# Optimization experiments

Measured on AMD Instinct MI355X. Metric: run time of the kernel, lower is better.

Reference implementation:

```python
import jax, jax.numpy as jnp
import numpy as np

ALPHA = 0.2  # leaky relu slope

def setup_inputs() -> dict:
    key = jax.random.key(0)
    k1, k2, k3, k4 = jax.random.split(key, 4)
    b, n, din, dout = 8, 2048, 256, 128
    x = jax.random.normal(k1, (b, n, din), dtype=jnp.float32)
    adj = jax.random.randint(k2, (b, n, n), 0, 2, dtype=jnp.int32)
    # xavier-ish scaling for params
    W = jax.random.normal(k3, (dout, din), dtype=jnp.float32) * (1.414 * (2.0 / (din + dout)) ** 0.5)
    a = jax.random.normal(k4, (2 * dout,), dtype=jnp.float32) * (1.414 * (2.0 / (2 * dout + 1)) ** 0.5)
    return {"x": x, "adj": adj, "W": W, "a": a}

def reference(x, adj, W, a):
    # x: [b, n, din]; W: [dout, din]; a: [2*dout]
    wh = jnp.einsum('bnd,od->bno', x, W)           # [b, n, dout]
    dout = W.shape[0]
    a_src, a_dst = a[:dout], a[dout:]
    # e_ij = leaky_relu(a_src . wh_i + a_dst . wh_j)  (decomposed, avoids O(n^2 * 2d) concat)
    e = (wh @ a_src)[:, :, None] + (wh @ a_dst)[:, None, :]  # [b, n, n]
    e = jnp.where(e >= 0, e, ALPHA * e)
    e = jnp.where(adj != 0, e, -jnp.inf)
    attention = jax.nn.softmax(e, axis=2)          # [b, n, n]
    out = jnp.einsum('bij,bjo->bio', attention, wh)  # [b, n, dout]
    return jax.nn.relu(out)
```

## Files before the change

### kernel.cpp

```cpp
#include <hip/hip_runtime.h>
#include <hip/hip_bf16.h>
#include <stdint.h>

#define GAT_ALPHA 0.2f
#define LOG2E 1.4426950408889634f

typedef __attribute__((ext_vector_type(8))) __bf16 bf16x8;
typedef __attribute__((ext_vector_type(4))) float f32x4;

union B8 {
  bf16x8 b;
  unsigned short u[8];
  int4 i4;
};

__device__ __forceinline__ unsigned short f2bf(float f) {
  unsigned int u = __float_as_uint(f);
  u += 0x7fffu + ((u >> 16) & 1u);
  return (unsigned short)(u >> 16);
}

__device__ __forceinline__ void dma16(const void* g, void* l) {
  __builtin_amdgcn_global_load_lds(
      (const __attribute__((address_space(1))) unsigned int*)g,
      (__attribute__((address_space(3))) unsigned int*)l, 16, 0, 0);
}

__global__ __launch_bounds__(256) void gat_pack(
    const int* __restrict__ adj, unsigned long long* __restrict__ mask) {
  const int tid = threadIdx.x;
  const int lane = tid & 63;
  const int wgl = (blockIdx.x * 256 + tid) >> 6;
  for (int it = wgl; it < 131072; it += 4096) {
    const size_t base = (size_t)it << 8;
    const int* p = adj + base + lane;
    int a0 = p[0], a1 = p[64], a2 = p[128], a3 = p[192];
    unsigned long long m0 = __ballot(a0 != 0);
    unsigned long long m1 = __ballot(a1 != 0);
    unsigned long long m2 = __ballot(a2 != 0);
    unsigned long long m3 = __ballot(a3 != 0);
    if (lane == 0) {
      unsigned long long* mp = mask + (base >> 6);
      mp[0] = m0; mp[1] = m1; mp[2] = m2; mp[3] = m3;
    }
  }
}

__global__ __launch_bounds__(256, 2) void gat_wh(
    const float* __restrict__ x, const float* __restrict__ W,
    const float* __restrict__ a, unsigned short* __restrict__ whTf,
    float* __restrict__ s_out, float* __restrict__ d_out) {
  __shared__ float X[32][260];
  __shared__ float Wt[128][68];
  const int tid = threadIdx.x;
  const int row0 = blockIdx.x * 32;
  {
    const int rr = tid >> 3;
    const int seg = (tid & 7) << 2;
    const float* xrow = x + (size_t)(row0 + rr) * 256;
#pragma unroll
    for (int it = 0; it < 8; ++it) {
      const int k = seg + it * 32;
      *(float4*)(&X[rr][k]) = *(const float4*)(xrow + k);
    }
  }
  const int lane32 = tid & 31;
  const int r0 = (tid >> 5) << 2;
  float acc[4][4];
#pragma unroll
  for (int m = 0; m < 4; ++m)
#pragma unroll
    for (int r = 0; r < 4; ++r) acc[m][r] = 0.f;

  for (int kc = 0; kc < 4; ++kc) {
    __syncthreads();
#pragma unroll
    for (int p = 0; p < 8; ++p) {
      const int f = p * 1024 + tid * 4;
      const int row = f >> 6, col = f & 63;
      *(float4*)(&Wt[row][col]) = *(const float4*)(W + row * 256 + kc * 64 + col);
    }
    __syncthreads();
    const int kb = kc << 6;
#pragma unroll
    for (int k4 = 0; k4 < 16; ++k4) {
      const int kk = k4 << 2;
      float4 xv[4], wv[4];
#pragma unroll
      for (int r = 0; r < 4; ++r) xv[r] = *(const float4*)(&X[r0 + r][kb + kk]);
#pragma unroll
      for (int m = 0; m < 4; ++m) wv[m] = *(const float4*)(&Wt[lane32 + 32 * m][kk]);
#pragma unroll
      for (int m = 0; m < 4; ++m)
#pragma unroll
        for (int r = 0; r < 4; ++r) {
          acc[m][r] = fmaf(wv[m].x, xv[r].x, acc[m][r]);
          acc[m][r] = fmaf(wv[m].y, xv[r].y, acc[m][r]);
          acc[m][r] = fmaf(wv[m].z, xv[r].z, acc[m][r]);
          acc[m][r] = fmaf(wv[m].w, xv[r].w, acc[m][r]);
        }
    }
  }
  float asrc[4], adst[4];
#pragma unroll
  for (int m = 0; m < 4; ++m) {
    asrc[m] = a[lane32 + 32 * m];
    adst[m] = a[128 + lane32 + 32 * m];
  }
  float sp[4], dp[4];
#pragma unroll
  for (int r = 0; r < 4; ++r) {
    sp[r] = acc[0][r] * asrc[0] + acc[1][r] * asrc[1] + acc[2][r] * asrc[2] + acc[3][r] * asrc[3];
    dp[r] = acc[0][r] * adst[0] + acc[1][r] * adst[1] + acc[2][r] * adst[2] + acc[3][r] * adst[3];
  }
#pragma unroll
  for (int off = 16; off >= 1; off >>= 1) {
#pragma unroll
    for (int r = 0; r < 4; ++r) {
      sp[r] += __shfl_xor(sp[r], off, 64);
      dp[r] += __shfl_xor(dp[r], off, 64);
    }
  }
  if (lane32 == 0) {
#pragma unroll
    for (int r = 0; r < 4; ++r) {
      s_out[row0 + r0 + r] = sp[r];
      d_out[row0 + r0 + r] = dp[r];
    }
  }
  const int b = row0 >> 11;
  const int jc = (row0 & 2047) >> 5;
  const int q = r0 >> 3;
  const int u0 = r0 & 7;
#pragma unroll
  for (int m = 0; m < 4; ++m) {
    const int o = lane32 + 32 * m;
    const int nt = o >> 4, m16 = o & 15;
    uint2 pk;
    pk.x = (unsigned int)f2bf(acc[m][0]) | ((unsigned int)f2bf(acc[m][1]) << 16);
    pk.y = (unsigned int)f2bf(acc[m][2]) | ((unsigned int)f2bf(acc[m][3]) << 16);
    const size_t addr = ((((size_t)b * 64 + jc) * 8 + nt) << 9) + ((m16 + 16 * q) << 3) + u0;
    *(uint2*)(whTf + addr) = pk;
  }
}

__global__ __launch_bounds__(256) void gat_attn(
    const unsigned int* __restrict__ mask32, const unsigned short* __restrict__ whTf,
    const float* __restrict__ s, const float* __restrict__ dvec,
    float* __restrict__ out) {
  __shared__ unsigned short vbuf[2][2][8][512];
  __shared__ unsigned int maskl[64][68];
  __shared__ float dl[2048];
  const int tid = threadIdx.x;
  const int wave = tid >> 6;
  const int lane = tid & 63;
  const int il = lane & 15;
  const int quad = lane >> 4;
  const int qo = quad << 3;
  const int b = blockIdx.x & 7;
  const int tile = blockIdx.x >> 3;
  const int rbase = tile * 64;
  {
    const float* dsrc = dvec + ((size_t)b << 11);
#pragma unroll
    for (int it = 0; it < 2; ++it) {
      const int idx = it * 1024 + tid * 4;
      *(float4*)(&dl[idx]) = *(const float4*)(dsrc + idx);
    }
  }
  {
    const unsigned int* msrc = mask32 + (((size_t)b << 11) + rbase) * 64;
    const int c4 = (tid & 15) << 2;
#pragma unroll
    for (int kk = 0; kk < 4; ++kk) {
      const int r = (tid >> 4) + kk * 16;
      *(int4*)(&maskl[r][c4]) = *(const int4*)(msrc + r * 64 + c4);
    }
  }
  const unsigned short* whTb = whTf + (((size_t)b * 64) << 12);
  {
#pragma unroll
    for (int h = 0; h < 2; ++h) {
      const int nt = wave * 2 + h;
      dma16(whTb + ((size_t)(0 * 8 + nt) << 9) + (lane << 3), &vbuf[0][0][nt][0]);
      dma16(whTb + ((size_t)(1 * 8 + nt) << 9) + (lane << 3), &vbuf[0][1][nt][0]);
    }
  }
  const int i = rbase + wave * 16 + il;
  const size_t browi = ((size_t)b << 11) + i;
  const float sv = s[browi];
  const int mrow = wave * 16 + il;

  f32x4 acc[8];
#pragma unroll
  for (int nt = 0; nt < 8; ++nt) acc[nt] = (f32x4){0.f, 0.f, 0.f, 0.f};
  float den = 0.f;
  __syncthreads();

#pragma unroll 2
  for (int T = 0; T < 32; ++T) {
    const int cur = T & 1, nxt = cur ^ 1;
    if (T < 31) {
#pragma unroll
      for (int h = 0; h < 2; ++h) {
        const int nt = wave * 2 + h;
        dma16(whTb + (((size_t)(2 * T + 2) * 8 + nt) << 9) + (lane << 3), &vbuf[nxt][0][nt][0]);
        dma16(whTb + (((size_t)(2 * T + 3) * 8 + nt) << 9) + (lane << 3), &vbuf[nxt][1][nt][0]);
      }
    }
#pragma unroll
    for (int c = 0; c < 2; ++c) {
      const int tt = 2 * T + c;
      const int j0 = tt * 32;
      const unsigned int mword = maskl[mrow][tt];
      const float4 d0 = *(const float4*)(&dl[j0 + qo]);
      const float4 d1 = *(const float4*)(&dl[j0 + qo + 4]);
      const float dd[8] = {d0.x, d0.y, d0.z, d0.w, d1.x, d1.y, d1.z, d1.w};
      B8 af[8];
#pragma unroll
      for (int nt = 0; nt < 8; ++nt)
        af[nt].i4 = *(const int4*)((const char*)&vbuf[cur][c][nt][0] + lane * 16);
      B8 pf;
#pragma unroll
      for (int u = 0; u < 8; ++u) {
        float e = sv + dd[u];
        e = fmaxf(e, GAT_ALPHA * e);
        float p = __builtin_amdgcn_exp2f(e * LOG2E);
        p = ((mword >> (qo + u)) & 1u) ? p : 0.f;
        den += p;
        pf.u[u] = f2bf(p);
      }
#pragma unroll
      for (int nt = 0; nt < 8; ++nt)
        acc[nt] = __builtin_amdgcn_mfma_f32_16x16x32_bf16(af[nt].b, pf.b, acc[nt], 0, 0, 0);
    }
    __syncthreads();
  }
  den += __shfl_xor(den, 16, 64);
  den += __shfl_xor(den, 32, 64);
  const float inv = 1.0f / den;
  float* op = out + browi * 128;
#pragma unroll
  for (int nt = 0; nt < 8; ++nt) {
    float4 v;
    v.x = fmaxf(acc[nt][0] * inv, 0.f);
    v.y = fmaxf(acc[nt][1] * inv, 0.f);
    v.z = fmaxf(acc[nt][2] * inv, 0.f);
    v.w = fmaxf(acc[nt][3] * inv, 0.f);
    *(float4*)(op + nt * 16 + quad * 4) = v;
  }
}

extern "C" void kernel_launch(void* const* d_in, const int* in_sizes, int n_in,
                              void* d_out, int out_size, void* d_ws, size_t ws_size,
                              hipStream_t stream) {
  const float* x = (const float*)d_in[0];
  const int* adj = (const int*)d_in[1];
  const float* W = (const float*)d_in[2];
  const float* a = (const float*)d_in[3];
  float* out = (float*)d_out;
  unsigned short* whTf = (unsigned short*)d_ws;
  unsigned long long* mask = (unsigned long long*)((char*)d_ws + (size_t)4 * 1024 * 1024);
  float* s = (float*)((char*)d_ws + (size_t)8 * 1024 * 1024);
  float* dv = s + 16384;
  gat_pack<<<1024, 256, 0, stream>>>(adj, mask);
  gat_wh<<<512, 256, 0, stream>>>(x, W, a, whTf, s, dv);
  gat_attn<<<256, 256, 0, stream>>>((const unsigned int*)mask, whTf, s, dv, out);
}
```

Baseline: 268.1 us.

## Compute Wh projection with bf16 MFMA and prescale scores by log2e

```diff
diff --git a/kernel.cpp b/kernel.cpp
--- a/kernel.cpp
+++ b/kernel.cpp
@@ -11,19 +11,14 @@
 union B8 {
   bf16x8 b;
   unsigned short u[8];
+  unsigned int w[4];
   int4 i4;
 };
 
-__device__ __forceinline__ unsigned short f2bf(float f) {
-  unsigned int u = __float_as_uint(f);
-  u += 0x7fffu + ((u >> 16) & 1u);
-  return (unsigned short)(u >> 16);
-}
-
-__device__ __forceinline__ void dma16(const void* g, void* l) {
-  __builtin_amdgcn_global_load_lds(
-      (const __attribute__((address_space(1))) unsigned int*)g,
-      (__attribute__((address_space(3))) unsigned int*)l, 16, 0, 0);
+__device__ __forceinline__ unsigned int pk2bf(float lo, float hi) {
+  union { __hip_bfloat162 h; unsigned int u; } cv;
+  cv.h = __float22bfloat162_rn(make_float2(lo, hi));
+  return cv.u;
 }
 
 __global__ __launch_bounds__(256) void gat_pack(
@@ -50,98 +45,102 @@
     const float* __restrict__ x, const float* __restrict__ W,
     const float* __restrict__ a, unsigned short* __restrict__ whTf,
     float* __restrict__ s_out, float* __restrict__ d_out) {
-  __shared__ float X[32][260];
-  __shared__ float Wt[128][68];
+  __shared__ unsigned short WF[8][4][512];
   const int tid = threadIdx.x;
-  const int row0 = blockIdx.x * 32;
-  {
-    const int rr = tid >> 3;
-    const int seg = (tid & 7) << 2;
-    const float* xrow = x + (size_t)(row0 + rr) * 256;
-#pragma unroll
-    for (int it = 0; it < 8; ++it) {
-      const int k = seg + it * 32;
-      *(float4*)(&X[rr][k]) = *(const float4*)(xrow + k);
-    }
-  }
-  const int lane32 = tid & 31;
-  const int r0 = (tid >> 5) << 2;
-  float acc[4][4];
-#pragma unroll
-  for (int m = 0; m < 4; ++m)
-#pragma unroll
-    for (int r = 0; r < 4; ++r) acc[m][r] = 0.f;
-
-  for (int kc = 0; kc < 4; ++kc) {
+  const int wave = tid >> 6, lane = tid & 63;
+  const int il = lane & 15, quad = lane >> 4;
+  const int row0 = blockIdx.x * 64;
+  const int i = row0 + wave * 16 + il;
+  B8 av[8];
+  {
+    const float* xp = x + (size_t)i * 256 + quad * 8;
+#pragma unroll
+    for (int kc = 0; kc < 8; ++kc) {
+      float4 lo = *(const float4*)(xp + kc * 32);
+      float4 hi = *(const float4*)(xp + kc * 32 + 4);
+      av[kc].w[0] = pk2bf(lo.x, lo.y);
+      av[kc].w[1] = pk2bf(lo.z, lo.w);
+      av[kc].w[2] = pk2bf(hi.x, hi.y);
+      av[kc].w[3] = pk2bf(hi.z, hi.w);
+    }
+  }
+  f32x4 acc[8];
+#pragma unroll
+  for (int nt = 0; nt < 8; ++nt) acc[nt] = (f32x4){0.f, 0.f, 0.f, 0.f};
+#pragma unroll
+  for (int h = 0; h < 2; ++h) {
+    if (h) __syncthreads();
+#pragma unroll
+    for (int p = 0; p < 16; ++p) {
+      const int f = p * 1024 + tid * 4;
+      const int o = f >> 7, kk = f & 127;
+      float4 v = *(const float4*)(W + o * 256 + h * 128 + kk);
+      uint2 pk;
+      pk.x = pk2bf(v.x, v.y);
+      pk.y = pk2bf(v.z, v.w);
+      *(uint2*)(&WF[o >> 4][kk >> 5][((o & 15) + (((kk & 31) >> 3) << 4)) * 8 + (kk & 7)]) = pk;
+    }
     __syncthreads();
 #pragma unroll
-    for (int p = 0; p < 8; ++p) {
-      const int f = p * 1024 + tid * 4;
-      const int row = f >> 6, col = f & 63;
-      *(float4*)(&Wt[row][col]) = *(const float4*)(W + row * 256 + kc * 64 + col);
-    }
-    __syncthreads();
-    const int kb = kc << 6;
-#pragma unroll
-    for (int k4 = 0; k4 < 16; ++k4) {
-      const int kk = k4 << 2;
-      float4 xv[4], wv[4];
-#pragma unroll
-      for (int r = 0; r < 4; ++r) xv[r] = *(const float4*)(&X[r0 + r][kb + kk]);
-#pragma unroll
-      for (int m = 0; m < 4; ++m) wv[m] = *(const float4*)(&Wt[lane32 + 32 * m][kk]);
-#pragma unroll
-      for (int m = 0; m < 4; ++m)
-#pragma unroll
-        for (int r = 0; r < 4; ++r) {
-          acc[m][r] = fmaf(wv[m].x, xv[r].x, acc[m][r]);
-          acc[m][r] = fmaf(wv[m].y, xv[r].y, acc[m][r]);
-          acc[m][r] = fmaf(wv[m].z, xv[r].z, acc[m][r]);
-          acc[m][r] = fmaf(wv[m].w, xv[r].w, acc[m][r]);
-        }
-    }
-  }
-  float asrc[4], adst[4];
-#pragma unroll
-  for (int m = 0; m < 4; ++m) {
-    asrc[m] = a[lane32 + 32 * m];
-    adst[m] = a[128 + lane32 + 32 * m];
+    for (int kl = 0; kl < 4; ++kl) {
+      const int kc = h * 4 + kl;
+#pragma unroll
+      for (int nt = 0; nt < 8; ++nt) {
+        B8 bv;
+        bv.i4 = *(const int4*)(&WF[nt][kl][lane * 8]);
+        acc[nt] = __builtin_amdgcn_mfma_f32_16x16x32_bf16(av[kc].b, bv.b, acc[nt], 0, 0, 0);
+      }
+    }
+  }
+  float asrc[8], adst[8];
+#pragma unroll
+  for (int nt = 0; nt < 8; ++nt) {
+    asrc[nt] = a[nt * 16 + il];
+    adst[nt] = a[128 + nt * 16 + il];
   }
   float sp[4], dp[4];
 #pragma unroll
   for (int r = 0; r < 4; ++r) {
-    sp[r] = acc[0][r] * asrc[0] + acc[1][r] * asrc[1] + acc[2][r] * asrc[2] + acc[3][r] * asrc[3];
-    dp[r] = acc[0][r] * adst[0] + acc[1][r] * adst[1] + acc[2][r] * adst[2] + acc[3][r] * adst[3];
-  }
-#pragma unroll
-  for (int off = 16; off >= 1; off >>= 1) {
+    float sv = 0.f, dv = 0.f;
+#pragma unroll
+    for (int nt = 0; nt < 8; ++nt) {
+      sv += acc[nt][r] * asrc[nt];
+      dv += acc[nt][r] * adst[nt];
+    }
+    sp[r] = sv; dp[r] = dv;
+  }
+#pragma unroll
+  for (int off = 1; off <= 8; off <<= 1) {
 #pragma unroll
     for (int r = 0; r < 4; ++r) {
       sp[r] += __shfl_xor(sp[r], off, 64);
       dp[r] += __shfl_xor(dp[r], off, 64);
     }
   }
-  if (lane32 == 0) {
+  if (il == 0) {
 #pragma unroll
     for (int r = 0; r < 4; ++r) {
-      s_out[row0 + r0 + r] = sp[r];
-      d_out[row0 + r0 + r] = dp[r];
+      s_out[row0 + wave * 16 + quad * 4 + r] = sp[r];
+      d_out[row0 + wave * 16 + quad * 4 + r] = dp[r];
     }
   }
   const int b = row0 >> 11;
-  const int jc = (row0 & 2047) >> 5;
-  const int q = r0 >> 3;
-  const int u0 = r0 & 7;
-#pragma unroll
-  for (int m = 0; m < 4; ++m) {
-    const int o = lane32 + 32 * m;
-    const int nt = o >> 4, m16 = o & 15;
+  const int jc = ((row0 & 2047) >> 5) + (wave >> 1);
+  const int kin = ((wave & 1) << 4) + (quad << 2);
+  const int kq = kin >> 3, u0 = kin & 7;
+#pragma unroll
+  for (int nt = 0; nt < 8; ++nt) {
     uint2 pk;
-    pk.x = (unsigned int)f2bf(acc[m][0]) | ((unsigned int)f2bf(acc[m][1]) << 16);
-    pk.y = (unsigned int)f2bf(acc[m][2]) | ((unsigned int)f2bf(acc[m][3]) << 16);
-    const size_t addr = ((((size_t)b * 64 + jc) * 8 + nt) << 9) + ((m16 + 16 * q) << 3) + u0;
-    *(uint2*)(whTf + addr) = pk;
-  }
+    pk.x = pk2bf(acc[nt][0], acc[nt][1]);
+    pk.y = pk2bf(acc[nt][2], acc[nt][3]);
+    *(uint2*)(whTf + ((((size_t)(b * 64 + jc)) * 8 + nt) << 9) + ((il + (kq << 4)) << 3) + u0) = pk;
+  }
+}
+
+__device__ __forceinline__ void dma16(const void* g, void* l) {
+  __builtin_amdgcn_global_load_lds(
+      (const __attribute__((address_space(1))) unsigned int*)g,
+      (__attribute__((address_space(3))) unsigned int*)l, 16, 0, 0);
 }
 
 __global__ __launch_bounds__(256) void gat_attn(
@@ -165,7 +164,9 @@
 #pragma unroll
     for (int it = 0; it < 2; ++it) {
       const int idx = it * 1024 + tid * 4;
-      *(float4*)(&dl[idx]) = *(const float4*)(dsrc + idx);
+      float4 v = *(const float4*)(dsrc + idx);
+      v.x *= LOG2E; v.y *= LOG2E; v.z *= LOG2E; v.w *= LOG2E;
+      *(float4*)(&dl[idx]) = v;
     }
   }
   {
@@ -188,7 +189,7 @@
   }
   const int i = rbase + wave * 16 + il;
   const size_t browi = ((size_t)b << 11) + i;
-  const float sv = s[browi];
+  const float svL = s[browi] * LOG2E;
   const int mrow = wave * 16 + il;
 
   f32x4 acc[8];
@@ -220,16 +221,21 @@
 #pragma unroll
       for (int nt = 0; nt < 8; ++nt)
         af[nt].i4 = *(const int4*)((const char*)&vbuf[cur][c][nt][0] + lane * 16);
-      B8 pf;
+      float pv[8];
 #pragma unroll
       for (int u = 0; u < 8; ++u) {
-        float e = sv + dd[u];
-        e = fmaxf(e, GAT_ALPHA * e);
-        float p = __builtin_amdgcn_exp2f(e * LOG2E);
+        float t0 = svL + dd[u];
+        float e2 = fmaxf(t0, GAT_ALPHA * t0);
+        float p = __builtin_amdgcn_exp2f(e2);
         p = ((mword >> (qo + u)) & 1u) ? p : 0.f;
         den += p;
-        pf.u[u] = f2bf(p);
+        pv[u] = p;
       }
+      B8 pf;
+      pf.w[0] = pk2bf(pv[0], pv[1]);
+      pf.w[1] = pk2bf(pv[2], pv[3]);
+      pf.w[2] = pk2bf(pv[4], pv[5]);
+      pf.w[3] = pk2bf(pv[6], pv[7]);
 #pragma unroll
       for (int nt = 0; nt < 8; ++nt)
         acc[nt] = __builtin_amdgcn_mfma_f32_16x16x32_bf16(af[nt].b, pf.b, acc[nt], 0, 0, 0);
@@ -264,6 +270,6 @@
   float* s = (float*)((char*)d_ws + (size_t)8 * 1024 * 1024);
   float* dv = s + 16384;
   gat_pack<<<1024, 256, 0, stream>>>(adj, mask);
-  gat_wh<<<512, 256, 0, stream>>>(x, W, a, whTf, s, dv);
+  gat_wh<<<256, 256, 0, stream>>>(x, W, a, whTf, s, dv);
   gat_attn<<<256, 256, 0, stream>>>((const unsigned int*)mask, whTf, s, dv, out);
 }
```

Result: faster. 255.5 us (-4.7%).
